# Performance work log

Hardware: AMD Instinct MI355X
Metric: run time of the kernel (lower is better)

Reference implementation:

```python
import jax, jax.numpy as jnp
import numpy as np

K = 32        # num_classes
NQ = 16384    # num query samples
C = 512       # feature_dim
H_REF = 512   # refinement_net hidden
H_CONF = 256  # confidence_net hidden
NUM_STEPS = 3


def setup_inputs() -> dict:
    key = jax.random.key(0)
    ks = jax.random.split(key, 8)
    s = 0.02
    return {
        "prototypes": jax.random.normal(ks[0], (K, C), jnp.float32),
        "query_features": jax.random.normal(ks[1], (NQ, C), jnp.float32),
        "query_distances": jax.random.uniform(ks[2], (NQ, K), jnp.float32) * 10.0,
        "W1": jax.random.normal(ks[3], (2 * C, H_REF), jnp.float32) * s,
        "b1": jnp.zeros((H_REF,), jnp.float32),
        "W2": jax.random.normal(ks[4], (H_REF, C), jnp.float32) * s,
        "b2": jnp.zeros((C,), jnp.float32),
        "Wc1": jax.random.normal(ks[5], (2 * C, H_CONF), jnp.float32) * s,
        "bc1": jnp.zeros((H_CONF,), jnp.float32),
        "Wc2": jax.random.normal(ks[6], (H_CONF, 1), jnp.float32) * s,
        "bc2": jnp.zeros((1,), jnp.float32),
    }


def reference(prototypes, query_features, query_distances,
              W1, b1, W2, b2, Wc1, bc1, Wc2, bc2):
    # ---- refinement loop (3 steps, sequential in refined prototypes) ----
    refined = prototypes
    for step in range(NUM_STEPS):
        # soft assignments over classes; temperature = step + 1
        soft = jax.nn.softmax(-query_distances / (step + 1.0), axis=-1)  # (NQ, K)
        wsum = jnp.maximum(soft.sum(axis=0), 1e-6)                       # (K,)  clamp(min=1e-6)
        wmean = (soft.T @ query_features) / wsum[:, None]                # (K, C)
        concat = jnp.concatenate([refined, wmean], axis=-1)              # (K, 2C)
        h = jax.nn.relu(concat @ W1 + b1)                                # dropout is identity in eval
        refinement = h @ W2 + b2                                         # (K, C)
        refined = refined + 0.1 * refinement

    # ---- confidence scores: MLP on [proto, query] pairs, mean over queries ----
    # Split first-layer weight into proto half and query half to avoid
    # materializing the (K, NQ, 2C) concat explicitly (same math).
    Wp, Wq = Wc1[:C], Wc1[C:]
    hp = prototypes @ Wp          # (K, H_CONF)
    hq = query_features @ Wq      # (NQ, H_CONF)
    hidden = jax.nn.relu(hp[:, None, :] + hq[None, :, :] + bc1)  # (K, NQ, H_CONF)
    conf = jax.nn.sigmoid(hidden @ Wc2 + bc2)                    # (K, NQ, 1)
    confidence_scores = conf.reshape(K, -1).mean(axis=1)         # (K,)

    return refined, confidence_scores
```

## Files before the change

kernel.cpp:

```cpp
#include <hip/hip_runtime.h>

#define KP 32
#define NQg 16384
#define CD 512
#define HC 256
#define NS 3

typedef __attribute__((ext_vector_type(8))) short short8;
typedef __attribute__((ext_vector_type(4))) short short4_t;
typedef __attribute__((ext_vector_type(8))) __bf16 bf16x8;
typedef __attribute__((ext_vector_type(4))) float floatx4;

union S8B8 { short8 s; bf16x8 b; };

__device__ __forceinline__ short f2bf(float f) {
    union { float f; unsigned u; } v; v.f = f;
    unsigned r = v.u + 0x7fffu + ((v.u >> 16) & 1u);
    return (short)(r >> 16);
}
__device__ __forceinline__ float bf2f(short s) {
    union { unsigned u; float f; } v; v.u = ((unsigned)(unsigned short)s) << 16;
    return v.f;
}
__device__ __forceinline__ float bflo(unsigned u) { return __uint_as_float(u << 16); }
__device__ __forceinline__ float bfhi(unsigned u) { return __uint_as_float(u & 0xffff0000u); }

__global__ __launch_bounds__(256) void k_A(const float* __restrict__ qd,
                                           const float* __restrict__ W1, const float* __restrict__ W2,
                                           const float* __restrict__ Wc1, const float* __restrict__ proto,
                                           const float* __restrict__ qf,
                                           short* __restrict__ softT,
                                           short* __restrict__ W1p, short* __restrict__ W2p,
                                           short* __restrict__ wqp, float* __restrict__ refined,
                                           short* __restrict__ qf2b, float* __restrict__ wmean,
                                           int* __restrict__ bar, float* __restrict__ dout) {
    int tid = threadIdx.x;
    int bid = blockIdx.x;
    if (bid < 64) {
        int q = bid * 256 + tid;
        float d[32];
        const float4* p = (const float4*)(qd + (size_t)q * 32);
#pragma unroll
        for (int j = 0; j < 8; j++) {
            float4 v = p[j];
            d[4 * j] = v.x; d[4 * j + 1] = v.y; d[4 * j + 2] = v.z; d[4 * j + 3] = v.w;
        }
#pragma unroll
        for (int s = 0; s < 3; s++) {
            float inv = -1.0f / (float)(s + 1);
            float e[32];
            float sum = 0.f;
#pragma unroll
            for (int k = 0; k < 32; k++) { e[k] = __expf(d[k] * inv); sum += e[k]; }
            float r = 1.0f / sum;
#pragma unroll
            for (int k = 0; k < 32; k++)
                softT[(size_t)(s * 32 + k) * NQg + q] = f2bf(e[k] * r);
        }
        return;
    }
    if (bid < 3712) {
        if (bid == 64) {
            if (tid < 32) dout[16384 + tid] = 0.f;
            else if (tid < 40) bar[tid - 32] = 0;
        }
        int idx = (bid - 64) * 256 + tid;
        if (idx < 524288) {
            int k = idx >> 9, n = idx & 511;
            W1p[((size_t)(k >> 3) * 512 + n) * 8 + (k & 7)] = f2bf(W1[idx]);
        } else if (idx < 786432) {
            int j = idx - 524288;
            int k = j >> 9, n = j & 511;
            W2p[((size_t)(k >> 3) * 512 + n) * 8 + (k & 7)] = f2bf(W2[j]);
        } else if (idx < 917504) {
            int j = idx - 786432;
            int k = j >> 8, n = j & 255;
            wqp[((size_t)(k >> 3) * 256 + n) * 8 + (k & 7)] = f2bf(Wc1[(size_t)(512 + k) * 256 + n]);
        } else {
            int j = idx - 917504;
            refined[j] = proto[j];
        }
        return;
    }
    if (bid < 3904) {
        int idx = (bid - 3712) * 256 + tid;
        wmean[idx] = 0.f;
        return;
    }
    {
        int j = (bid - 3904) * 256 + tid;
        float4 v = *(const float4*)&qf[(size_t)j * 4];
        short4_t o;
        o[0] = f2bf(v.x); o[1] = f2bf(v.y); o[2] = f2bf(v.z); o[3] = f2bf(v.w);
        *(short4_t*)&qf2b[(size_t)j * 4] = o;
    }
}

__global__ __launch_bounds__(256) void k_B(const short* __restrict__ qf2b,
                                           const short* __restrict__ softT,
                                           const short* __restrict__ wqp,
                                           float* __restrict__ wmean,
                                           short* __restrict__ hq_g,
                                           float* __restrict__ wsuminv,
                                           const float* __restrict__ proto,
                                           const float* __restrict__ Wc1,
                                           const float* __restrict__ bc1,
                                           float* __restrict__ hpb) {
    __shared__ short B_lds[128 * 40];
    int tid = threadIdx.x;
    int lane = tid & 63, w = tid >> 6;
    int ml = lane & 15, q8 = lane >> 4;

    if (blockIdx.x < 256) {
        int kc = blockIdx.x >> 2, ns = blockIdx.x & 3;
        int c0 = ns * 128;
        int qbase0 = kc * 256;
        int c_l = 2 * lane;
        int q_l = 8 * w;

        floatx4 acc[6][2];
#pragma unroll
        for (int mt = 0; mt < 6; mt++)
#pragma unroll
            for (int nt = 0; nt < 2; nt++) acc[mt][nt] = (floatx4){0.f, 0.f, 0.f, 0.f};

        for (int step = 0; step < 8; step++) {
            int qb = qbase0 + step * 32;
            short8 sA, sB;
#pragma unroll
            for (int i = 0; i < 8; i++) {
                unsigned u = *(const unsigned*)&qf2b[(size_t)(qb + q_l + i) * 512 + c0 + c_l];
                sA[i] = (short)(u & 0xffffu);
                sB[i] = (short)(u >> 16);
            }
            __syncthreads();
            *(short8*)&B_lds[c_l * 40 + q_l] = sA;
            *(short8*)&B_lds[(c_l + 1) * 40 + q_l] = sB;
            S8B8 a[6];
#pragma unroll
            for (int mt = 0; mt < 6; mt++)
                a[mt].s = *(const short8*)&softT[(size_t)(mt * 16 + ml) * NQg + qb + q8 * 8];
            __syncthreads();
#pragma unroll
            for (int nt = 0; nt < 2; nt++) {
                S8B8 b; b.s = *(short8*)&B_lds[(w * 32 + nt * 16 + ml) * 40 + q8 * 8];
#pragma unroll
                for (int mt = 0; mt < 6; mt++)
                    acc[mt][nt] = __builtin_amdgcn_mfma_f32_16x16x32_bf16(a[mt].b, b.b, acc[mt][nt], 0, 0, 0);
            }
        }
#pragma unroll
        for (int mt = 0; mt < 6; mt++) {
#pragma unroll
            for (int nt = 0; nt < 2; nt++) {
                int c = c0 + w * 32 + nt * 16 + ml;
#pragma unroll
                for (int r = 0; r < 4; r++) {
                    int m = mt * 16 + q8 * 4 + r;
                    atomicAdd(&wmean[(size_t)m * 512 + c], acc[mt][nt][r]);
                }
            }
        }
    } else if (blockIdx.x < 512) {
        int m0 = (blockIdx.x - 256) * 64;
        int n0 = w * 64;
        floatx4 acc[4][4];
#pragma unroll
        for (int mt = 0; mt < 4; mt++)
#pragma unroll
            for (int nt = 0; nt < 4; nt++) acc[mt][nt] = (floatx4){0.f, 0.f, 0.f, 0.f};

#pragma unroll 4
        for (int kc = 0; kc < 512; kc += 32) {
            S8B8 a[4], b[4];
#pragma unroll
            for (int mt = 0; mt < 4; mt++)
                a[mt].s = *(const short8*)&qf2b[(size_t)(m0 + mt * 16 + ml) * 512 + kc + q8 * 8];
#pragma unroll
            for (int nt = 0; nt < 4; nt++)
                b[nt].s = *(const short8*)&wqp[((size_t)((kc >> 3) + q8) * 256 + n0 + nt * 16 + ml) * 8];
#pragma unroll
            for (int mt = 0; mt < 4; mt++)
#pragma unroll
                for (int nt = 0; nt < 4; nt++)
                    acc[mt][nt] = __builtin_amdgcn_mfma_f32_16x16x32_bf16(a[mt].b, b[nt].b, acc[mt][nt], 0, 0, 0);
        }
#pragma unroll
        for (int mt = 0; mt < 4; mt++)
#pragma unroll
            for (int nt = 0; nt < 4; nt++) {
                int col = n0 + nt * 16 + ml;
#pragma unroll
                for (int r = 0; r < 4; r++) {
                    int row = m0 + mt * 16 + q8 * 4 + r;
                    hq_g[(size_t)row * 256 + col] = f2bf(acc[mt][nt][r]);
                }
            }
    } else if (blockIdx.x < 608) {
        float* red = (float*)B_lds;
        int sk = blockIdx.x - 512;
        const short* row = softT + (size_t)sk * NQg;
        float s = 0.f;
#pragma unroll
        for (int j = 0; j < 8; j++) {
            short8 v = *(const short8*)&row[j * 2048 + tid * 8];
#pragma unroll
            for (int i = 0; i < 8; i++) s += bf2f(v[i]);
        }
        red[tid] = s;
        __syncthreads();
        for (int off = 128; off > 0; off >>= 1) {
            if (tid < off) red[tid] += red[tid + off];
            __syncthreads();
        }
        if (tid == 0) wsuminv[sk] = 1.0f / fmaxf(red[0], 1e-6f);
    } else {
        int r = blockIdx.x - 608;
        const float* pr = proto + r * 512;
        const float* wc = Wc1 + tid;
        float a0 = 0.f, a1 = 0.f, a2 = 0.f, a3 = 0.f;
#pragma unroll 4
        for (int i = 0; i < 512; i += 4) {
            float4 p4 = *(const float4*)&pr[i];
            float w0 = wc[(size_t)i * 256];
            float w1 = wc[(size_t)(i + 1) * 256];
            float w2 = wc[(size_t)(i + 2) * 256];
            float w3 = wc[(size_t)(i + 3) * 256];
            a0 += p4.x * w0;
            a1 += p4.y * w1;
            a2 += p4.z * w2;
            a3 += p4.w * w3;
        }
        hpb[r * 256 + tid] = bc1[tid] + ((a0 + a1) + (a2 + a3));
    }
}

__device__ __forceinline__ void gbar(int* bar, int phase, int nblk) {
    __syncthreads();
    if (threadIdx.x == 0) {
        __threadfence();
        __hip_atomic_fetch_add(&bar[phase], 1, __ATOMIC_ACQ_REL, __HIP_MEMORY_SCOPE_AGENT);
        while (__hip_atomic_load(&bar[phase], __ATOMIC_ACQUIRE, __HIP_MEMORY_SCOPE_AGENT) < nblk)
            __builtin_amdgcn_s_sleep(1);
    }
    __syncthreads();
}

__global__ __launch_bounds__(256) void k_D(const float* __restrict__ wmean,
                                           const float* __restrict__ wsuminv,
                                           const short* __restrict__ W1p,
                                           const float* __restrict__ b1,
                                           const short* __restrict__ W2p,
                                           const float* __restrict__ b2,
                                           float* __restrict__ refined,
                                           short* __restrict__ hb,
                                           int* __restrict__ bar,
                                           const short* __restrict__ hq_g,
                                           const float* __restrict__ hpb,
                                           const float* __restrict__ Wc2,
                                           const float* __restrict__ bc2p,
                                           float* __restrict__ dout) {
    __shared__ float smem[6688];
    int tid = threadIdx.x, lane = tid & 63, w = tid >> 6;
    int ml = lane & 15, q8 = lane >> 4;

    if (blockIdx.x < 16) {
        float (*red)[32][36] = (float(*)[32][36])smem;
        int nb = blockIdx.x;
        int phase = 0;
        for (int s = 0; s < 3; s++) {
            {
                const float* srcA = (w < 2) ? refined : (wmean + (size_t)s * 32 * 512 - 512);
                float iv0 = 1.f, iv1 = 1.f;
                if (w >= 2) {
                    iv0 = wsuminv[s * 32 + ml];
                    iv1 = wsuminv[s * 32 + 16 + ml];
                }
                int kw = w * 256;
                floatx4 acc[2][2];
#pragma unroll
                for (int mt = 0; mt < 2; mt++)
#pragma unroll
                    for (int nt = 0; nt < 2; nt++) acc[mt][nt] = (floatx4){0.f, 0.f, 0.f, 0.f};
                for (int st = 0; st < 8; st++) {
                    int k0 = kw + st * 32 + q8 * 8;
                    S8B8 a[2];
#pragma unroll
                    for (int mt = 0; mt < 2; mt++) {
                        float sc = mt ? iv1 : iv0;
                        const float* p = &srcA[(size_t)(mt * 16 + ml) * 512 + k0];
                        float4 f0 = *(const float4*)p;
                        float4 f1 = *(const float4*)(p + 4);
                        short8 t;
                        t[0] = f2bf(f0.x * sc); t[1] = f2bf(f0.y * sc);
                        t[2] = f2bf(f0.z * sc); t[3] = f2bf(f0.w * sc);
                        t[4] = f2bf(f1.x * sc); t[5] = f2bf(f1.y * sc);
                        t[6] = f2bf(f1.z * sc); t[7] = f2bf(f1.w * sc);
                        a[mt].s = t;
                    }
#pragma unroll
                    for (int nt = 0; nt < 2; nt++) {
                        int n = nb * 32 + nt * 16 + ml;
                        S8B8 b; b.s = *(const short8*)&W1p[((size_t)(k0 >> 3) * 512 + n) * 8];
#pragma unroll
                        for (int mt = 0; mt < 2; mt++)
                            acc[mt][nt] = __builtin_amdgcn_mfma_f32_16x16x32_bf16(a[mt].b, b.b, acc[mt][nt], 0, 0, 0);
                    }
                }
                __syncthreads();
#pragma unroll
                for (int mt = 0; mt < 2; mt++)
#pragma unroll
                    for (int nt = 0; nt < 2; nt++)
#pragma unroll
                        for (int r = 0; r < 4; r++)
                            red[w][mt * 16 + q8 * 4 + r][nt * 16 + ml] = acc[mt][nt][r];
                __syncthreads();
                int m = tid >> 3, n0 = (tid & 7) * 4;
                short4_t o;
#pragma unroll
                for (int i = 0; i < 4; i++) {
                    float v = b1[nb * 32 + n0 + i];
#pragma unroll
                    for (int w4 = 0; w4 < 4; w4++) v += red[w4][m][n0 + i];
                    o[i] = f2bf(fmaxf(v, 0.f));
                }
                *(short4_t*)&hb[(size_t)m * 512 + nb * 32 + n0] = o;
            }
            gbar(bar, phase++, 16);
            {
                int kw = w * 128;
                floatx4 acc[2][2];
#pragma unroll
                for (int mt = 0; mt < 2; mt++)
#pragma unroll
                    for (int nt = 0; nt < 2; nt++) acc[mt][nt] = (floatx4){0.f, 0.f, 0.f, 0.f};
                for (int st = 0; st < 4; st++) {
                    int k0 = kw + st * 32 + q8 * 8;
                    S8B8 a[2];
#pragma unroll
                    for (int mt = 0; mt < 2; mt++)
                        a[mt].s = *(const short8*)&hb[(size_t)(mt * 16 + ml) * 512 + k0];
#pragma unroll
                    for (int nt = 0; nt < 2; nt++) {
                        int n = nb * 32 + nt * 16 + ml;
                        S8B8 b; b.s = *(const short8*)&W2p[((size_t)(k0 >> 3) * 512 + n) * 8];
#pragma unroll
                        for (int mt = 0; mt < 2; mt++)
                            acc[mt][nt] = __builtin_amdgcn_mfma_f32_16x16x32_bf16(a[mt].b, b.b, acc[mt][nt], 0, 0, 0);
                    }
                }
                __syncthreads();
#pragma unroll
                for (int mt = 0; mt < 2; mt++)
#pragma unroll
                    for (int nt = 0; nt < 2; nt++)
#pragma unroll
                        for (int r = 0; r < 4; r++)
                            red[w][mt * 16 + q8 * 4 + r][nt * 16 + ml] = acc[mt][nt][r];
                __syncthreads();
                int m = tid >> 3, n0 = (tid & 7) * 4;
#pragma unroll
                for (int i = 0; i < 4; i++) {
                    int c = nb * 32 + n0 + i;
                    float v = b2[c];
#pragma unroll
                    for (int w4 = 0; w4 < 4; w4++) v += red[w4][m][n0 + i];
                    float val = refined[(size_t)m * 512 + c] + 0.1f * v;
                    refined[(size_t)m * 512 + c] = val;
                    if (s == 2) dout[(size_t)m * 512 + c] = val;
                }
            }
            if (s < 2) gbar(bar, phase++, 16);
        }
    } else {
        short* hq_lds = (short*)smem;
        short* hp_s   = (short*)smem + 4480;
        float* wc2s   = smem + 6400;
        float* confl  = smem + 6656;
        int q0 = (blockIdx.x - 16) * 16;

        wc2s[tid] = Wc2[tid];
        if (tid < 32) confl[tid] = 0.f;
#pragma unroll
        for (int i = 0; i < 8; i++) {
            int idx = i * 256 + tid;
            int r = idx >> 6, c = (idx & 63) * 4;
            float4 v = *(const float4*)&hpb[r * 256 + c];
            short4_t o;
            o[0] = f2bf(v.x); o[1] = f2bf(v.y); o[2] = f2bf(v.z); o[3] = f2bf(v.w);
            *(short4_t*)&hp_s[r * 260 + c] = o;
        }
        {
            const short* hqs = hq_g + (size_t)q0 * 256;
            int r = tid >> 4, c = (tid & 15) * 16;
            *(short8*)&hq_lds[r * 280 + c] = *(const short8*)&hqs[r * 256 + c];
            *(short8*)&hq_lds[r * 280 + c + 8] = *(const short8*)&hqs[r * 256 + c + 8];
        }
        __syncthreads();

        int q = tid & 15, kg = tid >> 4;
        int k0 = kg, k1 = kg + 16;
        float s0 = 0.f, s1 = 0.f;
        for (int h = 0; h < 256; h += 4) {
            uint2 hv = *(uint2*)&hq_lds[q * 280 + h];
            float f0 = bflo(hv.x), f1 = bfhi(hv.x), f2 = bflo(hv.y), f3 = bfhi(hv.y);
            uint2 u0 = *(uint2*)&hp_s[k0 * 260 + h];
            uint2 u1 = *(uint2*)&hp_s[k1 * 260 + h];
            float4 wv = *(float4*)&wc2s[h];
            s0 += fmaxf(bflo(u0.x) + f0, 0.f) * wv.x;
            s0 += fmaxf(bfhi(u0.x) + f1, 0.f) * wv.y;
            s0 += fmaxf(bflo(u0.y) + f2, 0.f) * wv.z;
            s0 += fmaxf(bfhi(u0.y) + f3, 0.f) * wv.w;
            s1 += fmaxf(bflo(u1.x) + f0, 0.f) * wv.x;
            s1 += fmaxf(bfhi(u1.x) + f1, 0.f) * wv.y;
            s1 += fmaxf(bflo(u1.y) + f2, 0.f) * wv.z;
            s1 += fmaxf(bfhi(u1.y) + f3, 0.f) * wv.w;
        }
        float bc2 = bc2p[0];
        float v0 = 1.f / (1.f + __expf(-(s0 + bc2)));
        float v1 = 1.f / (1.f + __expf(-(s1 + bc2)));
        atomicAdd(&confl[k0], v0);
        atomicAdd(&confl[k1], v1);
        __syncthreads();
        if (tid < 32) atomicAdd(&dout[16384 + tid], confl[tid] * (1.0f / 16384.0f));
    }
}

extern "C" void kernel_launch(void* const* d_in, const int* in_sizes, int n_in,
                              void* d_out, int out_size, void* d_ws, size_t ws_size,
                              hipStream_t stream) {
    const float* proto = (const float*)d_in[0];
    const float* qf    = (const float*)d_in[1];
    const float* qd    = (const float*)d_in[2];
    const float* W1    = (const float*)d_in[3];
    const float* b1    = (const float*)d_in[4];
    const float* W2    = (const float*)d_in[5];
    const float* b2    = (const float*)d_in[6];
    const float* Wc1   = (const float*)d_in[7];
    const float* bc1   = (const float*)d_in[8];
    const float* Wc2   = (const float*)d_in[9];
    const float* bc2   = (const float*)d_in[10];
    float* out = (float*)d_out;

    float* ws = (float*)d_ws;
    short* softT   = (short*)ws;
    short* qf2b    = (short*)(ws + 786432);
    float* wmean   = ws + 4980736;
    float* refined = ws + 5029888;
    short* hb      = (short*)(ws + 5046272);
    short* W1p     = (short*)(ws + 5054464);
    short* W2p     = (short*)(ws + 5316608);
    short* wqp     = (short*)(ws + 5447680);
    float* hpb     = ws + 5513216;
    int*   bar     = (int*)(ws + 5521408);
    float* wsuminv = ws + 5521416;
    short* hq      = (short*)(ws + 5521536);

    k_A<<<12096, 256, 0, stream>>>(qd, W1, W2, Wc1, proto, qf, softT, W1p, W2p, wqp,
                                   refined, qf2b, wmean, bar, out);
    k_B<<<640, 256, 0, stream>>>(qf2b, softT, wqp, wmean, hq, wsuminv, proto, Wc1, bc1, hpb);
    k_D<<<1040, 256, 0, stream>>>(wmean, wsuminv, W1p, b1, W2p, b2, refined, hb, bar,
                                  hq, hpb, Wc2, bc2, out);
}
```

Baseline: 171.3 us.

## Run refinement MLP in a single block to drop the cross-block grid barriers

The three-step refinement MLP moves from 16 cooperating blocks synchronized by global atomic barriers to a single 256-thread block. Each wave now covers 128 output columns over the full K range, and the hidden activations stay in LDS rather than global memory. This removes the cross-block barriers, the split-K LDS reduction and the global round-trip for the hidden layer. In exchange one block does all the weight-streaming MFMA work serially, which could lengthen the critical path if that branch is slower than the confidence blocks running alongside it.

```diff
diff --git a/kernel.cpp b/kernel.cpp
--- a/kernel.cpp
+++ b/kernel.cpp
@@ -235,17 +235,6 @@
     }
 }
 
-__device__ __forceinline__ void gbar(int* bar, int phase, int nblk) {
-    __syncthreads();
-    if (threadIdx.x == 0) {
-        __threadfence();
-        __hip_atomic_fetch_add(&bar[phase], 1, __ATOMIC_ACQ_REL, __HIP_MEMORY_SCOPE_AGENT);
-        while (__hip_atomic_load(&bar[phase], __ATOMIC_ACQUIRE, __HIP_MEMORY_SCOPE_AGENT) < nblk)
-            __builtin_amdgcn_s_sleep(1);
-    }
-    __syncthreads();
-}
-
 __global__ __launch_bounds__(256) void k_D(const float* __restrict__ wmean,
                                            const float* __restrict__ wsuminv,
                                            const short* __restrict__ W1p,
@@ -253,42 +242,48 @@
                                            const short* __restrict__ W2p,
                                            const float* __restrict__ b2,
                                            float* __restrict__ refined,
-                                           short* __restrict__ hb,
-                                           int* __restrict__ bar,
                                            const short* __restrict__ hq_g,
                                            const float* __restrict__ hpb,
                                            const float* __restrict__ Wc2,
                                            const float* __restrict__ bc2p,
                                            float* __restrict__ dout) {
-    __shared__ float smem[6688];
+    __shared__ float smem[8320];
     int tid = threadIdx.x, lane = tid & 63, w = tid >> 6;
     int ml = lane & 15, q8 = lane >> 4;
 
-    if (blockIdx.x < 16) {
-        float (*red)[32][36] = (float(*)[32][36])smem;
-        int nb = blockIdx.x;
-        int phase = 0;
+    if (blockIdx.x == 0) {
+        short* hb_lds = (short*)smem;
+        int nbase = w * 128;
         for (int s = 0; s < 3; s++) {
-            {
-                const float* srcA = (w < 2) ? refined : (wmean + (size_t)s * 32 * 512 - 512);
-                float iv0 = 1.f, iv1 = 1.f;
-                if (w >= 2) {
-                    iv0 = wsuminv[s * 32 + ml];
-                    iv1 = wsuminv[s * 32 + 16 + ml];
-                }
-                int kw = w * 256;
-                floatx4 acc[2][2];
-#pragma unroll
-                for (int mt = 0; mt < 2; mt++)
-#pragma unroll
-                    for (int nt = 0; nt < 2; nt++) acc[mt][nt] = (floatx4){0.f, 0.f, 0.f, 0.f};
-                for (int st = 0; st < 8; st++) {
-                    int k0 = kw + st * 32 + q8 * 8;
-                    S8B8 a[2];
+            float iv0 = wsuminv[s * 32 + ml];
+            float iv1 = wsuminv[s * 32 + 16 + ml];
+            const float* wmn = wmean + (size_t)s * 32 * 512;
+            floatx4 acc[2][8];
+#pragma unroll
+            for (int mt = 0; mt < 2; mt++)
+#pragma unroll
+                for (int nt = 0; nt < 8; nt++) acc[mt][nt] = (floatx4){0.f, 0.f, 0.f, 0.f};
+#pragma unroll 4
+            for (int kk = 0; kk < 32; kk++) {
+                int kgl = kk * 32 + q8 * 8;
+                S8B8 a[2];
+                if (kk < 16) {
+#pragma unroll
+                    for (int mt = 0; mt < 2; mt++) {
+                        const float* p = &refined[(size_t)(mt * 16 + ml) * 512 + kgl];
+                        float4 f0 = *(const float4*)p;
+                        float4 f1 = *(const float4*)(p + 4);
+                        short8 t;
+                        t[0] = f2bf(f0.x); t[1] = f2bf(f0.y); t[2] = f2bf(f0.z); t[3] = f2bf(f0.w);
+                        t[4] = f2bf(f1.x); t[5] = f2bf(f1.y); t[6] = f2bf(f1.z); t[7] = f2bf(f1.w);
+                        a[mt].s = t;
+                    }
+                } else {
+                    int kw = kgl - 512;
 #pragma unroll
                     for (int mt = 0; mt < 2; mt++) {
                         float sc = mt ? iv1 : iv0;
-                        const float* p = &srcA[(size_t)(mt * 16 + ml) * 512 + k0];
+                        const float* p = &wmn[(size_t)(mt * 16 + ml) * 512 + kw];
                         float4 f0 = *(const float4*)p;
                         float4 f1 = *(const float4*)(p + 4);
                         short8 t;
@@ -298,87 +293,73 @@
                         t[6] = f2bf(f1.z * sc); t[7] = f2bf(f1.w * sc);
                         a[mt].s = t;
                     }
-#pragma unroll
-                    for (int nt = 0; nt < 2; nt++) {
-                        int n = nb * 32 + nt * 16 + ml;
-                        S8B8 b; b.s = *(const short8*)&W1p[((size_t)(k0 >> 3) * 512 + n) * 8];
-#pragma unroll
-                        for (int mt = 0; mt < 2; mt++)
-                            acc[mt][nt] = __builtin_amdgcn_mfma_f32_16x16x32_bf16(a[mt].b, b.b, acc[mt][nt], 0, 0, 0);
+                }
+#pragma unroll
+                for (int nt = 0; nt < 8; nt++) {
+                    int n = nbase + nt * 16 + ml;
+                    S8B8 b; b.s = *(const short8*)&W1p[((size_t)(kgl >> 3) * 512 + n) * 8];
+#pragma unroll
+                    for (int mt = 0; mt < 2; mt++)
+                        acc[mt][nt] = __builtin_amdgcn_mfma_f32_16x16x32_bf16(a[mt].b, b.b, acc[mt][nt], 0, 0, 0);
+                }
+            }
+            if (s > 0) __syncthreads();
+#pragma unroll
+            for (int mt = 0; mt < 2; mt++)
+#pragma unroll
+                for (int nt = 0; nt < 8; nt++) {
+                    int col = nbase + nt * 16 + ml;
+                    float bv = b1[col];
+#pragma unroll
+                    for (int r = 0; r < 4; r++) {
+                        int row = mt * 16 + q8 * 4 + r;
+                        hb_lds[row * 520 + col] = f2bf(fmaxf(acc[mt][nt][r] + bv, 0.f));
                     }
                 }
-                __syncthreads();
+            __syncthreads();
+            floatx4 acc2[2][8];
+#pragma unroll
+            for (int mt = 0; mt < 2; mt++)
+#pragma unroll
+                for (int nt = 0; nt < 8; nt++) acc2[mt][nt] = (floatx4){0.f, 0.f, 0.f, 0.f};
+#pragma unroll 4
+            for (int kk = 0; kk < 16; kk++) {
+                int k0 = kk * 32 + q8 * 8;
+                S8B8 a[2];
 #pragma unroll
                 for (int mt = 0; mt < 2; mt++)
-#pragma unroll
-                    for (int nt = 0; nt < 2; nt++)
-#pragma unroll
-                        for (int r = 0; r < 4; r++)
-                            red[w][mt * 16 + q8 * 4 + r][nt * 16 + ml] = acc[mt][nt][r];
-                __syncthreads();
-                int m = tid >> 3, n0 = (tid & 7) * 4;
-                short4_t o;
-#pragma unroll
-                for (int i = 0; i < 4; i++) {
-                    float v = b1[nb * 32 + n0 + i];
-#pragma unroll
-                    for (int w4 = 0; w4 < 4; w4++) v += red[w4][m][n0 + i];
-                    o[i] = f2bf(fmaxf(v, 0.f));
-                }
-                *(short4_t*)&hb[(size_t)m * 512 + nb * 32 + n0] = o;
-            }
-            gbar(bar, phase++, 16);
-            {
-                int kw = w * 128;
-                floatx4 acc[2][2];
-#pragma unroll
-                for (int mt = 0; mt < 2; mt++)
-#pragma unroll
-                    for (int nt = 0; nt < 2; nt++) acc[mt][nt] = (floatx4){0.f, 0.f, 0.f, 0.f};
-                for (int st = 0; st < 4; st++) {
-                    int k0 = kw + st * 32 + q8 * 8;
-                    S8B8 a[2];
+                    a[mt].s = *(short8*)&hb_lds[(mt * 16 + ml) * 520 + k0];
+#pragma unroll
+                for (int nt = 0; nt < 8; nt++) {
+                    int n = nbase + nt * 16 + ml;
+                    S8B8 b; b.s = *(const short8*)&W2p[((size_t)(k0 >> 3) * 512 + n) * 8];
 #pragma unroll
                     for (int mt = 0; mt < 2; mt++)
-                        a[mt].s = *(const short8*)&hb[(size_t)(mt * 16 + ml) * 512 + k0];
-#pragma unroll
-                    for (int nt = 0; nt < 2; nt++) {
-                        int n = nb * 32 + nt * 16 + ml;
-                        S8B8 b; b.s = *(const short8*)&W2p[((size_t)(k0 >> 3) * 512 + n) * 8];
-#pragma unroll
-                        for (int mt = 0; mt < 2; mt++)
-                            acc[mt][nt] = __builtin_amdgcn_mfma_f32_16x16x32_bf16(a[mt].b, b.b, acc[mt][nt], 0, 0, 0);
+                        acc2[mt][nt] = __builtin_amdgcn_mfma_f32_16x16x32_bf16(a[mt].b, b.b, acc2[mt][nt], 0, 0, 0);
+                }
+            }
+#pragma unroll
+            for (int mt = 0; mt < 2; mt++)
+#pragma unroll
+                for (int nt = 0; nt < 8; nt++) {
+                    int c = nbase + nt * 16 + ml;
+                    float bv = b2[c];
+#pragma unroll
+                    for (int r = 0; r < 4; r++) {
+                        int row = mt * 16 + q8 * 4 + r;
+                        float val = refined[(size_t)row * 512 + c] + 0.1f * (acc2[mt][nt][r] + bv);
+                        refined[(size_t)row * 512 + c] = val;
+                        if (s == 2) dout[(size_t)row * 512 + c] = val;
                     }
                 }
-                __syncthreads();
-#pragma unroll
-                for (int mt = 0; mt < 2; mt++)
-#pragma unroll
-                    for (int nt = 0; nt < 2; nt++)
-#pragma unroll
-                        for (int r = 0; r < 4; r++)
-                            red[w][mt * 16 + q8 * 4 + r][nt * 16 + ml] = acc[mt][nt][r];
-                __syncthreads();
-                int m = tid >> 3, n0 = (tid & 7) * 4;
-#pragma unroll
-                for (int i = 0; i < 4; i++) {
-                    int c = nb * 32 + n0 + i;
-                    float v = b2[c];
-#pragma unroll
-                    for (int w4 = 0; w4 < 4; w4++) v += red[w4][m][n0 + i];
-                    float val = refined[(size_t)m * 512 + c] + 0.1f * v;
-                    refined[(size_t)m * 512 + c] = val;
-                    if (s == 2) dout[(size_t)m * 512 + c] = val;
-                }
-            }
-            if (s < 2) gbar(bar, phase++, 16);
+            __syncthreads();
         }
     } else {
         short* hq_lds = (short*)smem;
         short* hp_s   = (short*)smem + 4480;
         float* wc2s   = smem + 6400;
         float* confl  = smem + 6656;
-        int q0 = (blockIdx.x - 16) * 16;
+        int q0 = (blockIdx.x - 1) * 16;
 
         wc2s[tid] = Wc2[tid];
         if (tid < 32) confl[tid] = 0.f;
@@ -448,7 +429,6 @@
     short* qf2b    = (short*)(ws + 786432);
     float* wmean   = ws + 4980736;
     float* refined = ws + 5029888;
-    short* hb      = (short*)(ws + 5046272);
     short* W1p     = (short*)(ws + 5054464);
     short* W2p     = (short*)(ws + 5316608);
     short* wqp     = (short*)(ws + 5447680);
@@ -460,6 +440,6 @@
     k_A<<<12096, 256, 0, stream>>>(qd, W1, W2, Wc1, proto, qf, softT, W1p, W2p, wqp,
                                    refined, qf2b, wmean, bar, out);
     k_B<<<640, 256, 0, stream>>>(qf2b, softT, wqp, wmean, hq, wsuminv, proto, Wc1, bc1, hpb);
-    k_D<<<1040, 256, 0, stream>>>(wmean, wsuminv, W1p, b1, W2p, b2, refined, hb, bar,
+    k_D<<<1025, 256, 0, stream>>>(wmean, wsuminv, W1p, b1, W2p, b2, refined,
                                   hq, hpb, Wc2, bc2, out);
 }
```

Measured after the change: 304.5 us. 1.78x slower.
